# Performance work log

Measured on AMD Instinct MI355X. Metric: run time of the kernel, lower is better.

## Reference

```python
import jax, jax.numpy as jnp
import numpy as np

B, L = 2, 1024
N_EMBD = 768
D_FF = 4 * N_EMBD
N_EXPERT = 8
TOPK = 2
N_PREDICT = 2
LB_COEF = 0.01
KL_COEF = 1.0


def setup_inputs() -> dict:
    key = jax.random.key(0)
    k0, k1, k2, k3, k4 = jax.random.split(key, 5)
    s = 0.02
    x = jax.random.normal(k0, (B, L, N_EMBD), dtype=jnp.float32)
    Wg_prior = jax.random.normal(k1, (N_EMBD, N_EXPERT), dtype=jnp.float32) * s
    Wg_post = jax.random.normal(k2, (N_EMBD, N_EXPERT), dtype=jnp.float32) * s
    W_fc = jax.random.normal(k3, (N_EXPERT, N_EMBD, D_FF), dtype=jnp.float32) * s
    W_proj = jax.random.normal(k4, (N_EXPERT, D_FF, N_EMBD), dtype=jnp.float32) * s
    return {"x": x, "Wg_prior": Wg_prior, "Wg_post": Wg_post, "W_fc": W_fc, "W_proj": W_proj}


def reference(x, Wg_prior, Wg_post, W_fc, W_proj):
    b, l, h = x.shape
    x_flat = x.reshape(-1, h)                              # [N, h], N = b*l
    prior_logits = x_flat @ Wg_prior                       # [N, E]

    # lookforward: shift by N_PREDICT, pad tail with last token (training path, l > n)
    n = N_PREDICT
    x_future = jnp.concatenate(
        [x[:, n:, :], jnp.broadcast_to(x[:, -1:, :], (b, n, h))], axis=1)
    posterior_logits = x_future.reshape(-1, h) @ Wg_post   # [N, E]
    router_logits = posterior_logits                       # train: route with posterior

    expert_weights = jax.nn.softmax(router_logits, axis=-1)          # [N, E]
    selected_weights, selected_experts = jax.lax.top_k(expert_weights, TOPK)
    selected_weights = selected_weights / selected_weights.sum(-1, keepdims=True)

    onehot = jax.nn.one_hot(selected_experts, N_EXPERT, dtype=x.dtype)  # [N, K, E]
    combine = (onehot * selected_weights[..., None]).sum(axis=1)        # [N, E]

    # dispatch/combine: loop over the small fixed expert set (structurally distinct weights)
    out = jnp.zeros_like(x_flat)
    for e in range(N_EXPERT):
        h1 = jnp.square(jax.nn.relu(x_flat @ W_fc[e]))     # [N, 4h] relu(x)^2
        out = out + combine[:, e:e + 1] * (h1 @ W_proj[e])
    x_new = out.reshape(b, l, h)

    # load-balance aux loss
    num_tokens = b * l
    counts = onehot.sum(axis=(0, 1))                       # tokens assigned per expert
    f = counts / (num_tokens * TOPK)
    P = expert_weights.mean(axis=0)
    lb_loss = N_EXPERT * (f * P).sum() * LB_COEF

    # KL(posterior || prior)
    prior_lp = jax.nn.log_softmax(prior_logits, axis=-1)
    post_lp = jax.nn.log_softmax(posterior_logits, axis=-1)
    kl = (jnp.exp(post_lp) * (post_lp - prior_lp)).sum(-1).mean() * KL_COEF

    aux_loss = lb_loss + kl
    return x_new, aux_loss
```

## Files before the change

kernel.cpp:

```cpp
#include <hip/hip_runtime.h>
#include <hip/hip_bf16.h>

typedef __attribute__((ext_vector_type(8))) short short8v;
typedef __attribute__((ext_vector_type(4))) float f32x4;
typedef __attribute__((ext_vector_type(4))) int int4v;

#define NTOK  2048
#define NEMBD 768
#define DFF   3072
#define NEXP  8
#define MAXSLOT 5120
#define NT1 24
#define NT2 6
#define MAXT1 40
#define MAXT2 80

#define WS_XBF   0
#define WS_GATES (WS_XBF + (size_t)NTOK*NEMBD*2)
#define WS_TE    (WS_GATES + NTOK*8*4)
#define WS_TW    (WS_TE + NTOK*2*4)
#define WS_KL    (WS_TW + NTOK*2*4)
#define WS_CTRL  (WS_KL + NTOK*4)
#define WS_STOK  (WS_CTRL + 2048)
#define WS_TSLOT (WS_STOK + MAXSLOT*4)
#define WS_WFCT  (WS_TSLOT + NTOK*2*4)
#define WS_WPT   (WS_WFCT + (size_t)NEXP*DFF*NEMBD*2)
#define WS_H     (WS_WPT + (size_t)NEXP*NEMBD*DFF*2)
#define WS_OBUF  WS_WFCT

__device__ __forceinline__ unsigned short f2bf(float f) {
    union { float f; unsigned u; } v; v.f = f;
    unsigned r = v.u + 0x7fffu + ((v.u >> 16) & 1u);
    return (unsigned short)(r >> 16);
}

__device__ __forceinline__ void gload16(const void* g, void* l) {
    __builtin_amdgcn_global_load_lds(
        (const __attribute__((address_space(1))) void*)g,
        (__attribute__((address_space(3))) void*)l, 16, 0, 0);
}

__global__ __launch_bounds__(256) void k_front(
    const float* __restrict__ x, const float* __restrict__ WgP, const float* __restrict__ WgQ,
    const float* __restrict__ Wfc, const float* __restrict__ Wpj,
    unsigned short* __restrict__ WfcT, unsigned short* __restrict__ WpT,
    unsigned short* __restrict__ xbf, float* __restrict__ gates,
    int* __restrict__ te, float* __restrict__ tw, float* __restrict__ kl_tok)
{
    __shared__ unsigned short sT[64][72];
    int tid = threadIdx.x;
    int bid = blockIdx.x;
    if (bid < NEXP * 12 * 48 + NEXP * 48 * 12) {
        const float* in; unsigned short* out; int R, C, tilesC;
        if (bid < NEXP * 12 * 48) { in = Wfc; out = WfcT; R = NEMBD; C = DFF; tilesC = 48; }
        else { bid -= NEXP * 12 * 48; in = Wpj; out = WpT; R = DFF; C = NEMBD; tilesC = 12; }
        int per = (R >> 6) * tilesC;
        int e = bid / per, rem = bid % per;
        int rt = rem / tilesC, ct = rem % tilesC;
        const float* src = in + ((size_t)e * R + rt * 64) * C + ct * 64;
        #pragma unroll
        for (int i = 0; i < 4; ++i) {
            int idx = tid + i * 256;
            int r = idx >> 4, c4 = idx & 15;
            float4 v = *(const float4*)&src[(size_t)r * C + c4 * 4];
            ushort4 o; o.x = f2bf(v.x); o.y = f2bf(v.y); o.z = f2bf(v.z); o.w = f2bf(v.w);
            *(ushort4*)&sT[r][c4 * 4] = o;
        }
        __syncthreads();
        unsigned short* dst = out + ((size_t)e * C + ct * 64) * R + rt * 64;
        #pragma unroll
        for (int i = 0; i < 2; ++i) {
            int idx = tid + i * 256;
            int oc = idx >> 3, j = idx & 7;
            unsigned short u[8];
            #pragma unroll
            for (int s = 0; s < 8; ++s) u[s] = sT[j * 8 + s][oc];
            *(int4v*)&dst[(size_t)oc * R + j * 8] = *(const int4v*)u;
        }
        return;
    }
    int rb = bid - (NEXP * 12 * 48 + NEXP * 48 * 12);
    int wave = tid >> 6, lane = tid & 63;
    int t = rb * 4 + wave;
    int b = t >> 10, l = t & 1023;
    int lf = l + 2; if (lf > 1023) lf = 1023;
    const float* xr = x + (size_t)t * NEMBD;
    const float* xf = x + (size_t)((b << 10) + lf) * NEMBD;
    int e = lane & 7, kg = lane >> 3;

    float accP = 0.f, accQ = 0.f;
    #pragma unroll 8
    for (int i = 0; i < 96; ++i) {
        int k = kg + 8 * i;
        accP += xr[k] * WgP[k * NEXP + e];
        accQ += xf[k] * WgQ[k * NEXP + e];
    }
    #pragma unroll
    for (int off = 8; off < 64; off <<= 1) {
        accP += __shfl_xor(accP, off);
        accQ += __shfl_xor(accQ, off);
    }
    float mq = accQ, mp = accP;
    #pragma unroll
    for (int off = 1; off < 8; off <<= 1) {
        mq = fmaxf(mq, __shfl_xor(mq, off));
        mp = fmaxf(mp, __shfl_xor(mp, off));
    }
    float gq = __expf(accQ - mq), gp = __expf(accP - mp);
    float se = gq, sp = gp;
    #pragma unroll
    for (int off = 1; off < 8; off <<= 1) {
        se += __shfl_xor(se, off);
        sp += __shfl_xor(sp, off);
    }
    float v0 = gq; int e0 = e;
    #pragma unroll
    for (int off = 1; off < 8; off <<= 1) {
        float ov = __shfl_xor(v0, off); int oe = __shfl_xor(e0, off);
        if (ov > v0 || (ov == v0 && oe < e0)) { v0 = ov; e0 = oe; }
    }
    float vx = (e == e0) ? -1.f : gq;
    float v1 = vx; int e1 = e;
    #pragma unroll
    for (int off = 1; off < 8; off <<= 1) {
        float ov = __shfl_xor(v1, off); int oe = __shfl_xor(e1, off);
        if (ov > v1 || (ov == v1 && oe < e1)) { v1 = ov; e1 = oe; }
    }
    float lq = (accQ - mq) - logf(se);
    float lp = (accP - mp) - logf(sp);
    float kl = __expf(lq) * (lq - lp);
    #pragma unroll
    for (int off = 1; off < 8; off <<= 1) kl += __shfl_xor(kl, off);

    if (lane < 8) gates[t * NEXP + e] = gq / se;
    if (lane == 0) {
        float s2 = v0 + v1;
        te[t * 2] = e0; te[t * 2 + 1] = e1;
        tw[t * 2] = v0 / s2; tw[t * 2 + 1] = v1 / s2;
        kl_tok[t] = kl;
    }
    const float4* xs4 = (const float4*)(x + (size_t)rb * 4 * NEMBD);
    ushort4* xd4 = (ushort4*)(xbf + (size_t)rb * 4 * NEMBD);
    for (int i = tid; i < 4 * NEMBD / 4; i += 256) {
        float4 v = xs4[i];
        ushort4 o;
        o.x = f2bf(v.x); o.y = f2bf(v.y); o.z = f2bf(v.z); o.w = f2bf(v.w);
        xd4[i] = o;
    }
}

__global__ __launch_bounds__(256) void k_sched(
    const int* __restrict__ te, int* __restrict__ ctrl,
    int* __restrict__ stok, int* __restrict__ tslot)
{
    __shared__ int cur[NEXP];
    __shared__ int cnt_s[NEXP];
    __shared__ int sOff[NEXP];
    int tid = threadIdx.x, lane = tid & 63;
    if (tid < NEXP) { cur[tid] = 0; cnt_s[tid] = 0; }
    for (int i = tid; i < MAXSLOT; i += 256) stok[i] = 0;
    __syncthreads();
    int cc[NEXP];
    #pragma unroll
    for (int e = 0; e < NEXP; ++e) cc[e] = 0;
    for (int i = tid; i < NTOK * 2; i += 256) {
        int e = te[i];
        #pragma unroll
        for (int q = 0; q < NEXP; ++q) cc[q] += (e == q) ? 1 : 0;
    }
    #pragma unroll
    for (int e = 0; e < NEXP; ++e) {
        int v = cc[e];
        #pragma unroll
        for (int off = 32; off; off >>= 1) v += __shfl_xor(v, off);
        if (lane == 0) atomicAdd(&cnt_s[e], v);
    }
    __syncthreads();
    if (tid == 0) {
        int off = 0, n1 = 0, n2 = 0;
        for (int e = 0; e < NEXP; ++e) {
            int cnt = cnt_s[e];
            ctrl[e] = cnt;
            ctrl[16 + e] = off; sOff[e] = off;
            int t128 = (cnt + 127) >> 7;
            for (int m = 0; m < t128; ++m)     ctrl[64 + n1++]  = (e << 16) | m;
            for (int m = 0; m < 2 * t128; ++m) ctrl[128 + n2++] = (e << 16) | m;
            off += t128 << 7;
        }
        ctrl[24] = off; ctrl[25] = n1; ctrl[26] = n2;
    }
    __syncthreads();
    for (int t = tid; t < NTOK; t += 256) {
        #pragma unroll
        for (int k = 0; k < 2; ++k) {
            int e = te[t * 2 + k];
            int s = atomicAdd(&cur[e], 1);
            int flat = sOff[e] + s;
            stok[flat] = t; tslot[t * 2 + k] = flat;
        }
    }
}

__global__ __launch_bounds__(256) void k_gemm1(
    const unsigned short* __restrict__ xbf, const unsigned short* __restrict__ WfcT,
    const int* __restrict__ ctrl, const int* __restrict__ slot_tok,
    unsigned short* __restrict__ H)
{
    int bx = blockIdx.x;
    int swz = (bx & 7) * (MAXT1 * NT1 / 8) + (bx >> 3);
    int nt = swz / MAXT1, tI = swz % MAXT1;
    if (tI >= ctrl[25]) return;
    int pk = ctrl[64 + tI];
    int e = pk >> 16, mt = pk & 0xffff;
    int base = ctrl[16 + e] + (mt << 7);

    __shared__ unsigned short sAB[2 * 128 * 64];
    unsigned short* sA = sAB;
    unsigned short* sB = sAB + 128 * 64;

    int tid = threadIdx.x, w = tid >> 6, lane = tid & 63;
    int wr = w >> 1, wc = w & 1;

    int swsub = (((lane & 7) ^ ((lane >> 3) & 7)) << 3);
    const unsigned short* wfc = WfcT + ((size_t)e * DFF + nt * 128) * NEMBD;
    const unsigned short* aptr[4]; const unsigned short* bptr[4];
    #pragma unroll
    for (int i = 0; i < 4; ++i) {
        int r = i * 32 + w * 8 + (lane >> 3);
        aptr[i] = xbf + (size_t)slot_tok[base + r] * NEMBD + swsub;
        bptr[i] = wfc + (size_t)r * NEMBD + swsub;
    }

    f32x4 acc[4][4];
    #pragma unroll
    for (int i = 0; i < 4; ++i)
        #pragma unroll
        for (int j = 0; j < 4; ++j) acc[i][j] = (f32x4){0.f, 0.f, 0.f, 0.f};

    int rsw = (lane & 7) << 3;
    for (int kk = 0; kk < NEMBD; kk += 64) {
        #pragma unroll
        for (int i = 0; i < 4; ++i) {
            gload16(aptr[i] + kk, &sA[(i * 256 + w * 64) * 8]);
            gload16(bptr[i] + kk, &sB[(i * 256 + w * 64) * 8]);
        }
        __syncthreads();
        #pragma unroll
        for (int kh = 0; kh < 2; ++kh) {
            int c = (kh * 32 + ((lane >> 4) << 3)) ^ rsw;
            short8v af[4], bfv[4];
            #pragma unroll
            for (int m = 0; m < 4; ++m)
                af[m] = *(const short8v*)&sA[(wr * 64 + m * 16 + (lane & 15)) * 64 + c];
            #pragma unroll
            for (int n = 0; n < 4; ++n)
                bfv[n] = *(const short8v*)&sB[(wc * 64 + n * 16 + (lane & 15)) * 64 + c];
            #pragma unroll
            for (int m = 0; m < 4; ++m)
                #pragma unroll
                for (int n = 0; n < 4; ++n)
                    acc[m][n] = __builtin_amdgcn_mfma_f32_16x16x32_bf16(af[m], bfv[n], acc[m][n], 0, 0, 0);
        }
        __syncthreads();
    }

    unsigned short* sC = sAB;
    #pragma unroll
    for (int m = 0; m < 4; ++m)
        #pragma unroll
        for (int n = 0; n < 4; ++n) {
            int col = wc * 64 + n * 16 + (lane & 15);
            #pragma unroll
            for (int i = 0; i < 4; ++i) {
                int row = wr * 64 + m * 16 + (lane >> 4) * 4 + i;
                float v = acc[m][n][i];
                v = v > 0.f ? v * v : 0.f;
                sC[row * 128 + col] = f2bf(v);
            }
        }
    __syncthreads();
    #pragma unroll
    for (int it = 0; it < 8; ++it) {
        int idx = tid + it * 256;
        int row = idx >> 4, j = idx & 15;
        *(int4v*)&H[(size_t)(base + row) * DFF + nt * 128 + j * 8] =
            *(const int4v*)&sC[row * 128 + j * 8];
    }
}

__global__ __launch_bounds__(256) void k_gemm2(
    const unsigned short* __restrict__ H, const unsigned short* __restrict__ WpT,
    const int* __restrict__ ctrl, float* __restrict__ obuf)
{
    int bx = blockIdx.x;
    int swz = (bx & 7) * (MAXT2 * NT2 / 8) + (bx >> 3);
    int nt = swz / MAXT2, tI = swz % MAXT2;
    if (tI >= ctrl[26]) return;
    int pk = ctrl[128 + tI];
    int e = pk >> 16, mt = pk & 0xffff;
    int base = ctrl[16 + e] + (mt << 6);

    __shared__ unsigned short sA[64 * 64];
    __shared__ unsigned short sB[128 * 64];

    int tid = threadIdx.x, w = tid >> 6, lane = tid & 63;
    int wr = w >> 1, wc = w & 1;

    int swsub = (((lane & 7) ^ ((lane >> 3) & 7)) << 3);
    const unsigned short* wp = WpT + ((size_t)e * NEMBD + nt * 128) * DFF;
    const unsigned short* aptr[2]; const unsigned short* bptr[4];
    #pragma unroll
    for (int i = 0; i < 2; ++i) {
        int r = i * 32 + w * 8 + (lane >> 3);
        aptr[i] = H + (size_t)(base + r) * DFF + swsub;
    }
    #pragma unroll
    for (int i = 0; i < 4; ++i) {
        int r = i * 32 + w * 8 + (lane >> 3);
        bptr[i] = wp + (size_t)r * DFF + swsub;
    }

    f32x4 acc[2][4];
    #pragma unroll
    for (int i = 0; i < 2; ++i)
        #pragma unroll
        for (int j = 0; j < 4; ++j) acc[i][j] = (f32x4){0.f, 0.f, 0.f, 0.f};

    int rsw = (lane & 7) << 3;
    for (int kk = 0; kk < DFF; kk += 64) {
        #pragma unroll
        for (int i = 0; i < 2; ++i)
            gload16(aptr[i] + kk, &sA[(i * 256 + w * 64) * 8]);
        #pragma unroll
        for (int i = 0; i < 4; ++i)
            gload16(bptr[i] + kk, &sB[(i * 256 + w * 64) * 8]);
        __syncthreads();
        #pragma unroll
        for (int kh = 0; kh < 2; ++kh) {
            int c = (kh * 32 + ((lane >> 4) << 3)) ^ rsw;
            short8v af[2], bfv[4];
            #pragma unroll
            for (int m = 0; m < 2; ++m)
                af[m] = *(const short8v*)&sA[(wr * 32 + m * 16 + (lane & 15)) * 64 + c];
            #pragma unroll
            for (int n = 0; n < 4; ++n)
                bfv[n] = *(const short8v*)&sB[(wc * 64 + n * 16 + (lane & 15)) * 64 + c];
            #pragma unroll
            for (int m = 0; m < 2; ++m)
                #pragma unroll
                for (int n = 0; n < 4; ++n)
                    acc[m][n] = __builtin_amdgcn_mfma_f32_16x16x32_bf16(af[m], bfv[n], acc[m][n], 0, 0, 0);
        }
        __syncthreads();
    }

    #pragma unroll
    for (int m = 0; m < 2; ++m)
        #pragma unroll
        for (int n = 0; n < 4; ++n) {
            int col = nt * 128 + wc * 64 + n * 16 + (lane & 15);
            #pragma unroll
            for (int i = 0; i < 4; ++i) {
                int row = wr * 32 + m * 16 + (lane >> 4) * 4 + i;
                obuf[(size_t)(base + row) * NEMBD + col] = acc[m][n][i];
            }
        }
}

__global__ __launch_bounds__(256) void k_finish(
    const float* __restrict__ obuf, const int* __restrict__ tslot,
    const float* __restrict__ tw, const float* __restrict__ gates,
    const float* __restrict__ kl_tok, const int* __restrict__ ctrl,
    float* __restrict__ out)
{
    int tid = threadIdx.x;
    if (blockIdx.x == 512) {
        __shared__ float sred[256];
        float p[NEXP]; float kls = 0.f;
        #pragma unroll
        for (int e = 0; e < NEXP; ++e) p[e] = 0.f;
        for (int t = tid; t < NTOK; t += 256) {
            #pragma unroll
            for (int e = 0; e < NEXP; ++e) p[e] += gates[t * NEXP + e];
            kls += kl_tok[t];
        }
        float Ps[NEXP];
        for (int e = 0; e < NEXP; ++e) {
            sred[tid] = p[e]; __syncthreads();
            for (int s = 128; s; s >>= 1) { if (tid < s) sred[tid] += sred[tid + s]; __syncthreads(); }
            if (tid == 0) Ps[e] = sred[0];
            __syncthreads();
        }
        sred[tid] = kls; __syncthreads();
        for (int s = 128; s; s >>= 1) { if (tid < s) sred[tid] += sred[tid + s]; __syncthreads(); }
        if (tid == 0) {
            float kl_mean = sred[0] / (float)NTOK;
            float lb = 0.f;
            for (int e = 0; e < NEXP; ++e)
                lb += ((float)ctrl[e] / (float)(NTOK * 2)) * (Ps[e] / (float)NTOK);
            lb *= (float)NEXP * 0.01f;
            out[(size_t)NTOK * NEMBD] = lb + kl_mean;
        }
        return;
    }
    int wave = tid >> 6, lane = tid & 63;
    int t = blockIdx.x * 4 + wave;
    int s0 = tslot[t * 2], s1 = tslot[t * 2 + 1];
    float g0 = tw[t * 2], g1 = tw[t * 2 + 1];
    const float4* r0 = (const float4*)(obuf + (size_t)s0 * NEMBD);
    const float4* r1 = (const float4*)(obuf + (size_t)s1 * NEMBD);
    float4* o4 = (float4*)(out + (size_t)t * NEMBD);
    #pragma unroll
    for (int j = 0; j < 3; ++j) {
        int c = j * 64 + lane;
        float4 a = r0[c], b = r1[c];
        float4 o;
        o.x = g0 * a.x + g1 * b.x; o.y = g0 * a.y + g1 * b.y;
        o.z = g0 * a.z + g1 * b.z; o.w = g0 * a.w + g1 * b.w;
        o4[c] = o;
    }
}

extern "C" void kernel_launch(void* const* d_in, const int* in_sizes, int n_in,
                              void* d_out, int out_size, void* d_ws, size_t ws_size,
                              hipStream_t stream) {
    const float* x   = (const float*)d_in[0];
    const float* WgP = (const float*)d_in[1];
    const float* WgQ = (const float*)d_in[2];
    const float* Wfc = (const float*)d_in[3];
    const float* Wpj = (const float*)d_in[4];
    float* out = (float*)d_out;

    char* ws = (char*)d_ws;
    unsigned short* xbf  = (unsigned short*)(ws + WS_XBF);
    float* gates = (float*)(ws + WS_GATES);
    int*   te    = (int*)(ws + WS_TE);
    float* tw    = (float*)(ws + WS_TW);
    float* klt   = (float*)(ws + WS_KL);
    int*   ctrl  = (int*)(ws + WS_CTRL);
    int*   stok  = (int*)(ws + WS_STOK);
    int*   tslot = (int*)(ws + WS_TSLOT);
    unsigned short* WfcT = (unsigned short*)(ws + WS_WFCT);
    unsigned short* WpT  = (unsigned short*)(ws + WS_WPT);
    unsigned short* H    = (unsigned short*)(ws + WS_H);
    float* obuf  = (float*)(ws + WS_OBUF);

    hipMemsetAsync(ctrl, 0, 64, stream);
    k_front<<<NEXP * 12 * 48 + NEXP * 48 * 12 + 512, 256, 0, stream>>>(
        x, WgP, WgQ, Wfc, Wpj, WfcT, WpT, xbf, gates, te, tw, klt);
    k_sched<<<1, 256, 0, stream>>>(te, ctrl, stok, tslot);
    k_gemm1<<<MAXT1 * NT1, 256, 0, stream>>>(xbf, WfcT, ctrl, stok, H);
    k_gemm2<<<MAXT2 * NT2, 256, 0, stream>>>(H, WpT, ctrl, obuf);
    k_finish<<<513, 256, 0, stream>>>(obuf, tslot, tw, gates, klt, ctrl, out);
}
```

Measured before the change: 174.8 us.

## Drop weight transpose; convert weights to bf16 in place and transpose B in LDS staging

The front kernel no longer transposes the expert weights through shared memory. It now does a straight fp32-to-bf16 conversion that keeps the original [K,N] layout. Both GEMM kernels stage the B tiles with register loads along K rows and scatter them transposed into swizzled LDS, replacing the async global-to-LDS loads. The memset of the control block is also removed. This cuts the cost of the transpose pass, but the GEMM B staging now runs synchronously through registers, which loses load overlap and adds LDS write work. Removing the memset may leave control state uninitialised.

```diff
diff --git a/kernel.cpp b/kernel.cpp
--- a/kernel.cpp
+++ b/kernel.cpp
@@ -2,6 +2,7 @@
 #include <hip/hip_bf16.h>
 
 typedef __attribute__((ext_vector_type(8))) short short8v;
+typedef __attribute__((ext_vector_type(4))) short short4v;
 typedef __attribute__((ext_vector_type(4))) float f32x4;
 typedef __attribute__((ext_vector_type(4))) int int4v;
 
@@ -23,10 +24,10 @@
 #define WS_CTRL  (WS_KL + NTOK*4)
 #define WS_STOK  (WS_CTRL + 2048)
 #define WS_TSLOT (WS_STOK + MAXSLOT*4)
-#define WS_WFCT  (WS_TSLOT + NTOK*2*4)
-#define WS_WPT   (WS_WFCT + (size_t)NEXP*DFF*NEMBD*2)
-#define WS_H     (WS_WPT + (size_t)NEXP*NEMBD*DFF*2)
-#define WS_OBUF  WS_WFCT
+#define WS_WFCB  (WS_TSLOT + NTOK*2*4)
+#define WS_WPB   (WS_WFCB + (size_t)NEXP*NEMBD*DFF*2)
+#define WS_H     (WS_WPB + (size_t)NEXP*DFF*NEMBD*2)
+#define WS_OBUF  WS_WFCB
 
 __device__ __forceinline__ unsigned short f2bf(float f) {
     union { float f; unsigned u; } v; v.f = f;
@@ -43,43 +44,31 @@
 __global__ __launch_bounds__(256) void k_front(
     const float* __restrict__ x, const float* __restrict__ WgP, const float* __restrict__ WgQ,
     const float* __restrict__ Wfc, const float* __restrict__ Wpj,
-    unsigned short* __restrict__ WfcT, unsigned short* __restrict__ WpT,
+    unsigned short* __restrict__ WfcB, unsigned short* __restrict__ WpB,
     unsigned short* __restrict__ xbf, float* __restrict__ gates,
     int* __restrict__ te, float* __restrict__ tw, float* __restrict__ kl_tok)
 {
-    __shared__ unsigned short sT[64][72];
     int tid = threadIdx.x;
     int bid = blockIdx.x;
-    if (bid < NEXP * 12 * 48 + NEXP * 48 * 12) {
-        const float* in; unsigned short* out; int R, C, tilesC;
-        if (bid < NEXP * 12 * 48) { in = Wfc; out = WfcT; R = NEMBD; C = DFF; tilesC = 48; }
-        else { bid -= NEXP * 12 * 48; in = Wpj; out = WpT; R = DFF; C = NEMBD; tilesC = 12; }
-        int per = (R >> 6) * tilesC;
-        int e = bid / per, rem = bid % per;
-        int rt = rem / tilesC, ct = rem % tilesC;
-        const float* src = in + ((size_t)e * R + rt * 64) * C + ct * 64;
-        #pragma unroll
-        for (int i = 0; i < 4; ++i) {
-            int idx = tid + i * 256;
-            int r = idx >> 4, c4 = idx & 15;
-            float4 v = *(const float4*)&src[(size_t)r * C + c4 * 4];
-            ushort4 o; o.x = f2bf(v.x); o.y = f2bf(v.y); o.z = f2bf(v.z); o.w = f2bf(v.w);
-            *(ushort4*)&sT[r][c4 * 4] = o;
-        }
-        __syncthreads();
-        unsigned short* dst = out + ((size_t)e * C + ct * 64) * R + rt * 64;
-        #pragma unroll
-        for (int i = 0; i < 2; ++i) {
-            int idx = tid + i * 256;
-            int oc = idx >> 3, j = idx & 7;
-            unsigned short u[8];
-            #pragma unroll
-            for (int s = 0; s < 8; ++s) u[s] = sT[j * 8 + s][oc];
-            *(int4v*)&dst[(size_t)oc * R + j * 8] = *(const int4v*)u;
+    if (bid >= 512) {
+        int cb = bid - 512;
+        const float* src; unsigned short* dst;
+        if (cb < 1024) { src = Wfc; dst = WfcB; }
+        else { cb -= 1024; src = Wpj; dst = WpB; }
+        const float4* s4 = (const float4*)src;
+        short8v* d8 = (short8v*)dst;
+        #pragma unroll
+        for (int u = 0; u < 9; ++u) {
+            int unit = cb * 2304 + u * 256 + tid;
+            float4 a = s4[unit * 2], b = s4[unit * 2 + 1];
+            short8v o;
+            o[0] = f2bf(a.x); o[1] = f2bf(a.y); o[2] = f2bf(a.z); o[3] = f2bf(a.w);
+            o[4] = f2bf(b.x); o[5] = f2bf(b.y); o[6] = f2bf(b.z); o[7] = f2bf(b.w);
+            d8[unit] = o;
         }
         return;
     }
-    int rb = bid - (NEXP * 12 * 48 + NEXP * 48 * 12);
+    int rb = bid;
     int wave = tid >> 6, lane = tid & 63;
     int t = rb * 4 + wave;
     int b = t >> 10, l = t & 1023;
@@ -201,8 +190,21 @@
     }
 }
 
+#define STAGE_B(sB, bbase, kk, Nstr) { \
+    const unsigned short* bs = (bbase) + (size_t)(kk) * (Nstr); \
+    short8v b0 = *(const short8v*)(bs); \
+    short8v b1 = *(const short8v*)(bs + (Nstr)); \
+    short8v b2 = *(const short8v*)(bs + 2 * (size_t)(Nstr)); \
+    short8v b3 = *(const short8v*)(bs + 3 * (size_t)(Nstr)); \
+    _Pragma("unroll") \
+    for (int j = 0; j < 8; ++j) { \
+        short4v v4 = (short4v){b0[j], b1[j], b2[j], b3[j]}; \
+        int elem = (ngg * 8 + j) * 64 + ((ko * 8) ^ (j << 3)) + klo; \
+        *(short4v*)&(sB)[elem] = v4; \
+    } }
+
 __global__ __launch_bounds__(256) void k_gemm1(
-    const unsigned short* __restrict__ xbf, const unsigned short* __restrict__ WfcT,
+    const unsigned short* __restrict__ xbf, const unsigned short* __restrict__ WfcB,
     const int* __restrict__ ctrl, const int* __restrict__ slot_tok,
     unsigned short* __restrict__ H)
 {
@@ -220,16 +222,18 @@
 
     int tid = threadIdx.x, w = tid >> 6, lane = tid & 63;
     int wr = w >> 1, wc = w & 1;
+    int kgg = tid & 15, ngg = tid >> 4;
+    int ko = kgg >> 1, klo = (kgg & 1) * 4;
 
     int swsub = (((lane & 7) ^ ((lane >> 3) & 7)) << 3);
-    const unsigned short* wfc = WfcT + ((size_t)e * DFF + nt * 128) * NEMBD;
-    const unsigned short* aptr[4]; const unsigned short* bptr[4];
+    const unsigned short* aptr[4];
     #pragma unroll
     for (int i = 0; i < 4; ++i) {
         int r = i * 32 + w * 8 + (lane >> 3);
         aptr[i] = xbf + (size_t)slot_tok[base + r] * NEMBD + swsub;
-        bptr[i] = wfc + (size_t)r * NEMBD + swsub;
-    }
+    }
+    const unsigned short* bbase = WfcB + (size_t)e * NEMBD * DFF + (size_t)(kgg * 4) * DFF
+                                + nt * 128 + ngg * 8;
 
     f32x4 acc[4][4];
     #pragma unroll
@@ -240,10 +244,9 @@
     int rsw = (lane & 7) << 3;
     for (int kk = 0; kk < NEMBD; kk += 64) {
         #pragma unroll
-        for (int i = 0; i < 4; ++i) {
+        for (int i = 0; i < 4; ++i)
             gload16(aptr[i] + kk, &sA[(i * 256 + w * 64) * 8]);
-            gload16(bptr[i] + kk, &sB[(i * 256 + w * 64) * 8]);
-        }
+        STAGE_B(sB, bbase, kk, DFF);
         __syncthreads();
         #pragma unroll
         for (int kh = 0; kh < 2; ++kh) {
@@ -289,7 +292,7 @@
 }
 
 __global__ __launch_bounds__(256) void k_gemm2(
-    const unsigned short* __restrict__ H, const unsigned short* __restrict__ WpT,
+    const unsigned short* __restrict__ H, const unsigned short* __restrict__ WpB,
     const int* __restrict__ ctrl, float* __restrict__ obuf)
 {
     int bx = blockIdx.x;
@@ -305,20 +308,18 @@
 
     int tid = threadIdx.x, w = tid >> 6, lane = tid & 63;
     int wr = w >> 1, wc = w & 1;
+    int kgg = tid & 15, ngg = tid >> 4;
+    int ko = kgg >> 1, klo = (kgg & 1) * 4;
 
     int swsub = (((lane & 7) ^ ((lane >> 3) & 7)) << 3);
-    const unsigned short* wp = WpT + ((size_t)e * NEMBD + nt * 128) * DFF;
-    const unsigned short* aptr[2]; const unsigned short* bptr[4];
+    const unsigned short* aptr[2];
     #pragma unroll
     for (int i = 0; i < 2; ++i) {
         int r = i * 32 + w * 8 + (lane >> 3);
         aptr[i] = H + (size_t)(base + r) * DFF + swsub;
     }
-    #pragma unroll
-    for (int i = 0; i < 4; ++i) {
-        int r = i * 32 + w * 8 + (lane >> 3);
-        bptr[i] = wp + (size_t)r * DFF + swsub;
-    }
+    const unsigned short* bbase = WpB + (size_t)e * DFF * NEMBD + (size_t)(kgg * 4) * NEMBD
+                                + nt * 128 + ngg * 8;
 
     f32x4 acc[2][4];
     #pragma unroll
@@ -331,9 +332,7 @@
         #pragma unroll
         for (int i = 0; i < 2; ++i)
             gload16(aptr[i] + kk, &sA[(i * 256 + w * 64) * 8]);
-        #pragma unroll
-        for (int i = 0; i < 4; ++i)
-            gload16(bptr[i] + kk, &sB[(i * 256 + w * 64) * 8]);
+        STAGE_B(sB, bbase, kk, NEMBD);
         __syncthreads();
         #pragma unroll
         for (int kh = 0; kh < 2; ++kh) {
@@ -440,16 +439,15 @@
     int*   ctrl  = (int*)(ws + WS_CTRL);
     int*   stok  = (int*)(ws + WS_STOK);
     int*   tslot = (int*)(ws + WS_TSLOT);
-    unsigned short* WfcT = (unsigned short*)(ws + WS_WFCT);
-    unsigned short* WpT  = (unsigned short*)(ws + WS_WPT);
+    unsigned short* WfcB = (unsigned short*)(ws + WS_WFCB);
+    unsigned short* WpB  = (unsigned short*)(ws + WS_WPB);
     unsigned short* H    = (unsigned short*)(ws + WS_H);
     float* obuf  = (float*)(ws + WS_OBUF);
 
-    hipMemsetAsync(ctrl, 0, 64, stream);
-    k_front<<<NEXP * 12 * 48 + NEXP * 48 * 12 + 512, 256, 0, stream>>>(
-        x, WgP, WgQ, Wfc, Wpj, WfcT, WpT, xbf, gates, te, tw, klt);
+    k_front<<<512 + 2048, 256, 0, stream>>>(
+        x, WgP, WgQ, Wfc, Wpj, WfcB, WpB, xbf, gates, te, tw, klt);
     k_sched<<<1, 256, 0, stream>>>(te, ctrl, stok, tslot);
-    k_gemm1<<<MAXT1 * NT1, 256, 0, stream>>>(xbf, WfcT, ctrl, stok, H);
-    k_gemm2<<<MAXT2 * NT2, 256, 0, stream>>>(H, WpT, ctrl, obuf);
+    k_gemm1<<<MAXT1 * NT1, 256, 0, stream>>>(xbf, WfcB, ctrl, stok, H);
+    k_gemm2<<<MAXT2 * NT2, 256, 0, stream>>>(H, WpB, ctrl, obuf);
     k_finish<<<513, 256, 0, stream>>>(obuf, tslot, tw, gates, klt, ctrl, out);
 }
```

Measured after the change: 192.6 us. +10.2%, slower.
